# Performance work log

Hardware: AMD Instinct MI355X
Metric: run time of the kernel (lower is better)

The kernel has to match this reference:

```python
import jax, jax.numpy as jnp
import numpy as np

B, LENGTH, D, IN = 32, 32, 384, 384
NCELLS = LENGTH * (LENGTH + 1) // 2  # 528

def _offsets():
    off = np.zeros(LENGTH, dtype=np.int64)
    for lvl in range(1, LENGTH):
        off[lvl] = off[lvl - 1] + (LENGTH - (lvl - 1))
    return off

_OFF = _offsets()

def _inside_index(level):
    Ls = LENGTH - level
    pos = np.arange(Ls)[:, None]
    k = np.arange(level)[None, :]
    left = _OFF[k] + pos                      # span (k, pos)
    right = _OFF[level - k - 1] + pos + k + 1  # span (level-k-1, pos+k+1)
    return jnp.asarray(left), jnp.asarray(right)

def _outside_index(level):
    Ls = LENGTH - level
    N = LENGTH - level - 1  # constant #contexts per position
    par = np.zeros((Ls, N), dtype=np.int64)
    sib = np.zeros((Ls, N), dtype=np.int64)
    for pos in range(Ls):
        j = 0
        for s in range(LENGTH - pos - level - 1):  # node is left child
            par[pos, j] = _OFF[level + s + 1] + pos
            sib[pos, j] = _OFF[s] + pos + level + 1
            j += 1
        for s in range(pos):  # node is right child
            par[pos, j] = _OFF[level + s + 1] + pos - s - 1
            sib[pos, j] = _OFF[s] + pos - s - 1
            j += 1
    return jnp.asarray(par), jnp.asarray(sib)

def sigma_h(x):
    return x * jnp.tanh(jnp.sqrt(jax.nn.sigmoid(x)))

def layer_norm(x, g, b, eps=1e-5):
    mu = x.mean(-1, keepdims=True)
    var = ((x - mu) ** 2).mean(-1, keepdims=True)
    return (x - mu) * jax.lax.rsqrt(var + eps) * g + b

def compose(l, r, W0, W1, B0, W2, B1):
    h = sigma_h(l @ W0 + r @ W1 + B0)
    return sigma_h(h @ W2 + B1)

def bilinear(u, v, M):
    return jnp.einsum('blnd,de,blne->bln', u, M, v)[..., None]

def setup_inputs() -> dict:
    key = jax.random.key(0)
    ks = jax.random.split(key, 16)
    sc = 1.0 / np.sqrt(D)
    mk = lambda k, shp: (jax.random.normal(k, shp, dtype=jnp.float32) * sc)
    inp = {
        'x': jax.random.normal(ks[0], (B, LENGTH, IN), dtype=jnp.float32),
        'leaf_W': mk(ks[1], (IN, D)), 'leaf_b': jnp.zeros((D,), jnp.float32),
        'in_ln_g': jnp.ones((D,), jnp.float32), 'in_ln_b': jnp.zeros((D,), jnp.float32),
        'out_ln_g': jnp.ones((D,), jnp.float32), 'out_ln_b': jnp.zeros((D,), jnp.float32),
        'root_h': jax.random.normal(ks[2], (D,), dtype=jnp.float32) * 0.02,
        'in_bi': mk(ks[3], (D, D)), 'out_bi': mk(ks[4], (D, D)),
        'in_W0': mk(ks[5], (D, D)), 'in_W1': mk(ks[6], (D, D)),
        'in_B0': jnp.zeros((D,), jnp.float32),
        'in_W2': mk(ks[7], (D, D)), 'in_B1': jnp.zeros((D,), jnp.float32),
        'out_W0': mk(ks[8], (D, D)), 'out_W1': mk(ks[9], (D, D)),
        'out_B0': jnp.zeros((D,), jnp.float32),
        'out_W2': mk(ks[10], (D, D)), 'out_B1': jnp.zeros((D,), jnp.float32),
    }
    return inp

def reference(x, leaf_W, leaf_b, in_ln_g, in_ln_b, out_ln_g, out_ln_b, root_h,
              in_bi, out_bi, in_W0, in_W1, in_B0, in_W2, in_B1,
              out_W0, out_W1, out_B0, out_W2, out_B1):
    # leaf transform
    h0 = layer_norm(sigma_h(x @ leaf_W + leaf_b), in_ln_g, in_ln_b)
    ih = jnp.zeros((B, NCELLS, D), x.dtype).at[:, :LENGTH].set(h0)
    is_ = jnp.zeros((B, NCELLS, 1), x.dtype)
    # inside pass (CKY chart, level-by-level)
    for level in range(1, LENGTH):
        li, ri = _inside_index(level)
        lh, rh = ih[:, li], ih[:, ri]   # [B, Ls, level, D]
        ls, rs = is_[:, li], is_[:, ri]
        sc = bilinear(lh, rh, in_bi) + ls + rs
        p = jax.nn.softmax(sc, axis=2)
        xc = compose(lh, rh, in_W0, in_W1, in_B0, in_W2, in_B1)
        hbar = layer_norm((p * xc).sum(2), in_ln_g, in_ln_b)
        sbar = (p * sc).sum(2)
        o = int(_OFF[level]); Ls = LENGTH - level
        ih = ih.at[:, o:o + Ls].set(hbar)
        is_ = is_.at[:, o:o + Ls].set(sbar)
    # outside pass
    oh = jnp.zeros((B, NCELLS, D), x.dtype)
    os_ = jnp.zeros((B, NCELLS, 1), x.dtype)
    root = layer_norm(jnp.broadcast_to(root_h, (B, 1, D)), out_ln_g, out_ln_b)
    oh = oh.at[:, -1:].set(root)
    for level in range(LENGTH - 2, -1, -1):
        pi, si = _outside_index(level)
        ph, sh = oh[:, pi], ih[:, si]   # parent outside / sibling inside
        ps, ss = os_[:, pi], is_[:, si]
        sc = bilinear(sh, ph, out_bi) + ss + ps
        p = jax.nn.softmax(sc, axis=2)
        xc = compose(ph, sh, out_W0, out_W1, out_B0, out_W2, out_B1)
        hbar = layer_norm((p * xc).sum(2), out_ln_g, out_ln_b)
        sbar = (p * sc).sum(2)
        o = int(_OFF[level]); Ls = LENGTH - level
        oh = oh.at[:, o:o + Ls].set(hbar)
        os_ = os_.at[:, o:o + Ls].set(sbar)
    return ih, is_, oh, os_
```

## Files before the change

### kernel.cpp

```cpp
#include <hip/hip_runtime.h>
#include <cstddef>

#define BDIM 32
#define LEN 32
#define DD 384
#define NCELLS 528

typedef _Float16 h16;
typedef __attribute__((ext_vector_type(8))) _Float16 v8h;
typedef __attribute__((ext_vector_type(4))) float v4f;

__device__ __forceinline__ int offf(int k) { return k * 32 - ((k * (k - 1)) >> 1); }
static inline int offh(int k) { return k * 32 - ((k * (k - 1)) >> 1); }

__device__ __forceinline__ float sigma_h_f(float x) {
  float s = 1.0f / (1.0f + __expf(-x));
  float r = sqrtf(s);
  float e2 = __expf(2.0f * r);
  float th = 1.0f - 2.0f / (e2 + 1.0f);
  return x * th;
}

__device__ __forceinline__ size_t rowbase(int r, int gLs, int gOff) {
  if (gLs == 0) return (size_t)r;
  int b = r / gLs;
  int p = r - b * gLs;
  return (size_t)b * NCELLS + gOff + p;
}

__global__ __launch_bounds__(256) void pack3_k(
    const float* __restrict__ w0, const float* __restrict__ w1,
    const float* __restrict__ bi, const float* __restrict__ ow1,
    const float* __restrict__ obi, const float* __restrict__ w2,
    const float* __restrict__ ow2, const float* __restrict__ ow0,
    const float* __restrict__ lw,
    float* __restrict__ WCt, float* __restrict__ W2t, float* __restrict__ OW2t,
    float* __restrict__ OW0t, float* __restrict__ LWt,
    float* __restrict__ isp, float* __restrict__ osp) {
  int i = blockIdx.x * 256 + threadIdx.x;
  if (i < 1920 * 384) {
    int n = i / 384, k = i - n * 384;
    int sel = n / 384, c = n - sel * 384;
    const float* src = sel == 0 ? w0 : sel == 1 ? w1 : sel == 2 ? bi
                       : sel == 3 ? ow1 : obi;
    WCt[i] = src[k * 384 + c];
  }
  if (i < 384 * 384) {
    int n = i / 384, k = i - n * 384;
    W2t[i]  = w2[k * 384 + n];
    OW2t[i] = ow2[k * 384 + n];
    OW0t[i] = ow0[k * 384 + n];
    LWt[i]  = lw[k * 384 + n];
  }
  if (i < BDIM * NCELLS) { isp[i] = 0.0f; osp[i] = 0.0f; }
}

__global__ __launch_bounds__(256) void gemm32s(
    const float* __restrict__ A, const float* __restrict__ Wt,
    const float* __restrict__ bias, float* __restrict__ C,
    int M, int N, int act, int gLs, int gOff) {
  __shared__ h16 Ah[64][40], Al[64][40];
  __shared__ h16 Bh[128][40], Bl[128][40];
  int tid = threadIdx.x;
  int w = tid >> 6, lane = tid & 63;
  int m0 = blockIdx.x * 64, n0 = blockIdx.y * 128;
  int r = lane & 15, q = lane >> 4;

  v4f acc[4][2];
#pragma unroll
  for (int i = 0; i < 4; ++i)
#pragma unroll
    for (int j = 0; j < 2; ++j) acc[i][j] = (v4f){0.f, 0.f, 0.f, 0.f};

  int sar = tid >> 2;
  int sak = (tid & 3) << 3;
  const float* Aptr = nullptr;
  if (m0 + sar < M) Aptr = A + rowbase(m0 + sar, gLs, gOff) * (size_t)DD;
  int sbc = tid >> 1;
  int sbk = (tid & 1) << 4;
  const float* Bptr = Wt + (size_t)(n0 + sbc) * DD;

  for (int k0 = 0; k0 < DD; k0 += 32) {
    float4 a0 = make_float4(0.f, 0.f, 0.f, 0.f), a1 = a0;
    if (Aptr) {
      a0 = *reinterpret_cast<const float4*>(Aptr + k0 + sak);
      a1 = *reinterpret_cast<const float4*>(Aptr + k0 + sak + 4);
    }
    float4 b0 = *reinterpret_cast<const float4*>(Bptr + k0 + sbk);
    float4 b1 = *reinterpret_cast<const float4*>(Bptr + k0 + sbk + 4);
    float4 b2 = *reinterpret_cast<const float4*>(Bptr + k0 + sbk + 8);
    float4 b3 = *reinterpret_cast<const float4*>(Bptr + k0 + sbk + 12);
    __syncthreads();
    {
      float av[8] = {a0.x, a0.y, a0.z, a0.w, a1.x, a1.y, a1.z, a1.w};
      v8h hi, lo;
#pragma unroll
      for (int t = 0; t < 8; ++t) {
        h16 h = (h16)av[t];
        hi[t] = h;
        lo[t] = (h16)(av[t] - (float)h);
      }
      *reinterpret_cast<v8h*>(&Ah[sar][sak]) = hi;
      *reinterpret_cast<v8h*>(&Al[sar][sak]) = lo;
    }
    {
      float bv[16] = {b0.x, b0.y, b0.z, b0.w, b1.x, b1.y, b1.z, b1.w,
                      b2.x, b2.y, b2.z, b2.w, b3.x, b3.y, b3.z, b3.w};
      v8h hi0, lo0, hi1, lo1;
#pragma unroll
      for (int t = 0; t < 8; ++t) {
        h16 h = (h16)bv[t];
        hi0[t] = h;
        lo0[t] = (h16)(bv[t] - (float)h);
      }
#pragma unroll
      for (int t = 0; t < 8; ++t) {
        h16 h = (h16)bv[8 + t];
        hi1[t] = h;
        lo1[t] = (h16)(bv[8 + t] - (float)h);
      }
      *reinterpret_cast<v8h*>(&Bh[sbc][sbk]) = hi0;
      *reinterpret_cast<v8h*>(&Bl[sbc][sbk]) = lo0;
      *reinterpret_cast<v8h*>(&Bh[sbc][sbk + 8]) = hi1;
      *reinterpret_cast<v8h*>(&Bl[sbc][sbk + 8]) = lo1;
    }
    __syncthreads();
    v8h afh[4], afl[4], bfh[2], bfl[2];
#pragma unroll
    for (int i = 0; i < 4; ++i) {
      afh[i] = *reinterpret_cast<const v8h*>(&Ah[i * 16 + r][q * 8]);
      afl[i] = *reinterpret_cast<const v8h*>(&Al[i * 16 + r][q * 8]);
    }
#pragma unroll
    for (int j = 0; j < 2; ++j) {
      bfh[j] = *reinterpret_cast<const v8h*>(&Bh[w * 32 + j * 16 + r][q * 8]);
      bfl[j] = *reinterpret_cast<const v8h*>(&Bl[w * 32 + j * 16 + r][q * 8]);
    }
#pragma unroll
    for (int i = 0; i < 4; ++i)
#pragma unroll
      for (int j = 0; j < 2; ++j) {
        acc[i][j] = __builtin_amdgcn_mfma_f32_16x16x32_f16(afl[i], bfh[j], acc[i][j], 0, 0, 0);
        acc[i][j] = __builtin_amdgcn_mfma_f32_16x16x32_f16(afh[i], bfl[j], acc[i][j], 0, 0, 0);
        acc[i][j] = __builtin_amdgcn_mfma_f32_16x16x32_f16(afh[i], bfh[j], acc[i][j], 0, 0, 0);
      }
  }

#pragma unroll
  for (int i = 0; i < 4; ++i) {
#pragma unroll
    for (int reg = 0; reg < 4; ++reg) {
      int rr = m0 + i * 16 + q * 4 + reg;
      if (rr >= M) continue;
      size_t cb = rowbase(rr, gLs, gOff) * (size_t)N;
#pragma unroll
      for (int j = 0; j < 2; ++j) {
        int col = n0 + w * 32 + j * 16 + r;
        float v = acc[i][j][reg];
        if (bias) v += bias[col];
        if (act) v = sigma_h_f(v);
        C[cb + col] = v;
      }
    }
  }
}

__global__ __launch_bounds__(256) void k1_in(
    const float* __restrict__ PC, const float* __restrict__ ihp,
    float* __restrict__ isp, float* __restrict__ H, float* __restrict__ Pw,
    const float* __restrict__ B0, int L, int Ls, int offL) {
  int g = blockIdx.x;
  int b = g / Ls, pos = g - b * Ls;
  int tid = threadIdx.x, lane = tid & 63, wv = tid >> 6;
  __shared__ float scs[32];
  size_t cb = (size_t)b * NCELLS;
  for (int n = wv; n < L; n += 4) {
    int lc = offf(n) + pos;
    int rc = offf(L - 1 - n) + pos + n + 1;
    const float* u = PC + (cb + lc) * 1920 + 768;
    const float* v = ihp + (cb + rc) * (size_t)DD;
    float s = 0.0f;
#pragma unroll
    for (int jj = 0; jj < 6; ++jj) s += u[lane + 64 * jj] * v[lane + 64 * jj];
#pragma unroll
    for (int o = 32; o; o >>= 1) s += __shfl_xor(s, o, 64);
    if (lane == 0) scs[n] = s + isp[cb + lc] + isp[cb + rc];
  }
  __syncthreads();
  if (wv == 0) {
    float v = (lane < L) ? scs[lane] : -3.0e38f;
    float m = v;
#pragma unroll
    for (int o = 32; o; o >>= 1) m = fmaxf(m, __shfl_xor(m, o, 64));
    float e = (lane < L) ? __expf(v - m) : 0.0f;
    float S = e;
#pragma unroll
    for (int o = 32; o; o >>= 1) S += __shfl_xor(S, o, 64);
    float pn = e / S;
    if (lane < L) Pw[(size_t)g * L + lane] = pn;
    float sb = (lane < L) ? pn * v : 0.0f;
#pragma unroll
    for (int o = 32; o; o >>= 1) sb += __shfl_xor(sb, o, 64);
    if (lane == 0) isp[cb + offL + pos] = sb;
  }
  for (int n = 0; n < L; ++n) {
    int lc = offf(n) + pos;
    int rc = offf(L - 1 - n) + pos + n + 1;
    const float* A0r = PC + (cb + lc) * 1920;
    const float* A1r = PC + (cb + rc) * 1920 + 384;
    float* hrow = H + ((size_t)g * L + n) * DD;
    for (int k = tid; k < DD; k += 256)
      hrow[k] = sigma_h_f(A0r[k] + A1r[k] + B0[k]);
  }
}

__global__ __launch_bounds__(256) void k1_out(
    const float* __restrict__ PC, const float* __restrict__ P0,
    const float* __restrict__ ohp, const float* __restrict__ isp,
    float* __restrict__ osp, float* __restrict__ H, float* __restrict__ Pw,
    const float* __restrict__ B0, int L, int Ls, int Nc, int offL) {
  int g = blockIdx.x;
  int b = g / Ls, pos = g - b * Ls;
  int tid = threadIdx.x, lane = tid & 63, wv = tid >> 6;
  __shared__ float scs[32];
  size_t cb = (size_t)b * NCELLS;
  int cnt0 = 31 - pos - L;
  for (int j = wv; j < Nc; j += 4) {
    int par, sib;
    if (j < cnt0) { par = offf(L + j + 1) + pos; sib = offf(j) + pos + L + 1; }
    else { int s2 = j - cnt0; par = offf(L + s2 + 1) + pos - s2 - 1; sib = offf(s2) + pos - s2 - 1; }
    const float* u = PC + (cb + sib) * 1920 + 1536;
    const float* v = ohp + (cb + par) * (size_t)DD;
    float s = 0.0f;
#pragma unroll
    for (int jj = 0; jj < 6; ++jj) s += u[lane + 64 * jj] * v[lane + 64 * jj];
#pragma unroll
    for (int o = 32; o; o >>= 1) s += __shfl_xor(s, o, 64);
    if (lane == 0) scs[j] = s + isp[cb + sib] + osp[cb + par];
  }
  __syncthreads();
  if (wv == 0) {
    float v = (lane < Nc) ? scs[lane] : -3.0e38f;
    float m = v;
#pragma unroll
    for (int o = 32; o; o >>= 1) m = fmaxf(m, __shfl_xor(m, o, 64));
    float e = (lane < Nc) ? __expf(v - m) : 0.0f;
    float S = e;
#pragma unroll
    for (int o = 32; o; o >>= 1) S += __shfl_xor(S, o, 64);
    float pn = e / S;
    if (lane < Nc) Pw[(size_t)g * Nc + lane] = pn;
    float sb = (lane < Nc) ? pn * v : 0.0f;
#pragma unroll
    for (int o = 32; o; o >>= 1) sb += __shfl_xor(sb, o, 64);
    if (lane == 0) osp[cb + offL + pos] = sb;
  }
  for (int j = 0; j < Nc; ++j) {
    int par, sib;
    if (j < cnt0) { par = offf(L + j + 1) + pos; sib = offf(j) + pos + L + 1; }
    else { int s2 = j - cnt0; par = offf(L + s2 + 1) + pos - s2 - 1; sib = offf(s2) + pos - s2 - 1; }
    const float* p0r = P0 + (cb + par) * (size_t)DD;
    const float* s1r = PC + (cb + sib) * 1920 + 1152;
    float* hrow = H + ((size_t)g * Nc + j) * DD;
    for (int k = tid; k < DD; k += 256)
      hrow[k] = sigma_h_f(p0r[k] + s1r[k] + B0[k]);
  }
}

__global__ __launch_bounds__(128) void k3_red_ln(
    const float* __restrict__ XC, const float* __restrict__ Pw,
    const float* __restrict__ lng, const float* __restrict__ lnb,
    float* __restrict__ outArr, int L, int Ls, int offL) {
  int g = blockIdx.x;
  int b = g / Ls, pos = g - b * Ls;
  int tid = threadIdx.x;
  float a0 = 0, a1 = 0, a2 = 0;
  const float* base = XC + (size_t)g * L * DD;
  for (int n = 0; n < L; ++n) {
    float pw = Pw ? Pw[(size_t)g * L + n] : 1.0f;
    const float* row = base + (size_t)n * DD;
    a0 += pw * row[tid];
    a1 += pw * row[tid + 128];
    a2 += pw * row[tid + 256];
  }
  int lane = tid & 63, wv = tid >> 6;
  float s = a0 + a1 + a2;
#pragma unroll
  for (int o = 32; o; o >>= 1) s += __shfl_xor(s, o, 64);
  __shared__ float r1[2], r2[2];
  if (lane == 0) r1[wv] = s;
  __syncthreads();
  float mean = (r1[0] + r1[1]) * (1.0f / 384.0f);
  float d0 = a0 - mean, d1 = a1 - mean, d2 = a2 - mean;
  float q = d0 * d0 + d1 * d1 + d2 * d2;
#pragma unroll
  for (int o = 32; o; o >>= 1) q += __shfl_xor(q, o, 64);
  if (lane == 0) r2[wv] = q;
  __syncthreads();
  float var = (r2[0] + r2[1]) * (1.0f / 384.0f);
  float inv = rsqrtf(var + 1e-5f);
  float* out = outArr + ((size_t)b * NCELLS + offL + pos) * DD;
  out[tid]       = d0 * inv * lng[tid]       + lnb[tid];
  out[tid + 128] = d1 * inv * lng[tid + 128] + lnb[tid + 128];
  out[tid + 256] = d2 * inv * lng[tid + 256] + lnb[tid + 256];
}

__global__ __launch_bounds__(384) void root_k(
    const float* __restrict__ rooth, const float* __restrict__ lng,
    const float* __restrict__ lnb, const float* __restrict__ W0,
    float* __restrict__ ohp, float* __restrict__ P0) {
  int tid = threadIdx.x;
  int lane = tid & 63, wv = tid >> 6;
  __shared__ float rl[384];
  __shared__ float r1[6], r2[6];
  float x = rooth[tid];
  float s = x;
#pragma unroll
  for (int o = 32; o; o >>= 1) s += __shfl_xor(s, o, 64);
  if (lane == 0) r1[wv] = s;
  __syncthreads();
  float mean = (r1[0] + r1[1] + r1[2] + r1[3] + r1[4] + r1[5]) * (1.0f / 384.0f);
  float d = x - mean;
  float q = d * d;
#pragma unroll
  for (int o = 32; o; o >>= 1) q += __shfl_xor(q, o, 64);
  if (lane == 0) r2[wv] = q;
  __syncthreads();
  float var = (r2[0] + r2[1] + r2[2] + r2[3] + r2[4] + r2[5]) * (1.0f / 384.0f);
  float inv = rsqrtf(var + 1e-5f);
  float v = d * inv * lng[tid] + lnb[tid];
  rl[tid] = v;
  __syncthreads();
  for (int b2 = 0; b2 < BDIM; ++b2)
    ohp[((size_t)b2 * NCELLS + 527) * DD + tid] = v;
  float acc = 0.0f;
  for (int d2 = 0; d2 < 384; ++d2) acc += rl[d2] * W0[(size_t)d2 * 384 + tid];
  for (int b2 = 0; b2 < BDIM; ++b2)
    P0[((size_t)b2 * NCELLS + 527) * DD + tid] = acc;
}

extern "C" void kernel_launch(void* const* d_in, const int* in_sizes, int n_in,
                              void* d_out, int out_size, void* d_ws, size_t ws_size,
                              hipStream_t stream) {
  const float* x        = (const float*)d_in[0];
  const float* leaf_W   = (const float*)d_in[1];
  const float* leaf_b   = (const float*)d_in[2];
  const float* in_ln_g  = (const float*)d_in[3];
  const float* in_ln_b  = (const float*)d_in[4];
  const float* out_ln_g = (const float*)d_in[5];
  const float* out_ln_b = (const float*)d_in[6];
  const float* root_h   = (const float*)d_in[7];
  const float* in_bi    = (const float*)d_in[8];
  const float* out_bi   = (const float*)d_in[9];
  const float* in_W0    = (const float*)d_in[10];
  const float* in_W1    = (const float*)d_in[11];
  const float* in_B0    = (const float*)d_in[12];
  const float* in_W2    = (const float*)d_in[13];
  const float* in_B1    = (const float*)d_in[14];
  const float* out_W0   = (const float*)d_in[15];
  const float* out_W1   = (const float*)d_in[16];
  const float* out_B0   = (const float*)d_in[17];
  const float* out_W2   = (const float*)d_in[18];
  const float* out_B1   = (const float*)d_in[19];

  float* ih  = (float*)d_out;
  float* isp = ih + (size_t)BDIM * NCELLS * DD;
  float* oh  = isp + (size_t)BDIM * NCELLS;
  float* osp = oh + (size_t)BDIM * NCELLS * DD;

  float* PC   = (float*)d_ws;
  float* P0   = PC + (size_t)BDIM * NCELLS * 1920;
  float* XCb  = P0 + (size_t)BDIM * NCELLS * 384;
  float* Hbuf = XCb + (size_t)31744 * 384;
  float* Pw   = Hbuf + (size_t)31744 * 384;
  float* WCt  = Pw + 31744;
  float* W2t  = WCt + (size_t)1920 * 384;
  float* OW2t = W2t + (size_t)384 * 384;
  float* OW0t = OW2t + (size_t)384 * 384;
  float* LWt  = OW0t + (size_t)384 * 384;

  pack3_k<<<2880, 256, 0, stream>>>(in_W0, in_W1, in_bi, out_W1, out_bi,
                                    in_W2, out_W2, out_W0, leaf_W,
                                    WCt, W2t, OW2t, OW0t, LWt, isp, osp);

  gemm32s<<<dim3(16, 3), 256, 0, stream>>>(x, LWt, leaf_b, XCb, 1024, 384, 1, 0, 0);
  k3_red_ln<<<1024, 128, 0, stream>>>(XCb, nullptr, in_ln_g, in_ln_b, ih, 1, 32, 0);
  gemm32s<<<dim3(16, 15), 256, 0, stream>>>(ih, WCt, nullptr, PC, 1024, 1920, 0, 32, 0);

  for (int L = 1; L < LEN; ++L) {
    int Ls = LEN - L, G = BDIM * Ls, M = G * L, off = offh(L);
    k1_in<<<G, 256, 0, stream>>>(PC, ih, isp, Hbuf, Pw, in_B0, L, Ls, off);
    gemm32s<<<dim3((M + 63) / 64, 3), 256, 0, stream>>>(Hbuf, W2t, in_B1, XCb, M, 384, 1, 0, 0);
    k3_red_ln<<<G, 128, 0, stream>>>(XCb, Pw, in_ln_g, in_ln_b, ih, L, Ls, off);
    gemm32s<<<dim3((G + 63) / 64, 15), 256, 0, stream>>>(ih, WCt, nullptr, PC, G, 1920, 0, Ls, off);
  }

  root_k<<<1, 384, 0, stream>>>(root_h, out_ln_g, out_ln_b, out_W0, oh, P0);

  for (int L = LEN - 2; L >= 0; --L) {
    int Ls = LEN - L, Nc = LEN - 1 - L, G = BDIM * Ls, M = G * Nc, off = offh(L);
    k1_out<<<G, 256, 0, stream>>>(PC, P0, oh, isp, osp, Hbuf, Pw, out_B0, L, Ls, Nc, off);
    gemm32s<<<dim3((M + 63) / 64, 3), 256, 0, stream>>>(Hbuf, OW2t, out_B1, XCb, M, 384, 1, 0, 0);
    k3_red_ln<<<G, 128, 0, stream>>>(XCb, Pw, out_ln_g, out_ln_b, oh, Nc, Ls, off);
    if (L > 0)
      gemm32s<<<dim3((G + 63) / 64, 3), 256, 0, stream>>>(oh, OW0t, nullptr, P0, G, 384, 0, Ls, off);
  }
}
```

Baseline: 5.101 ms.

## Pre-split GEMM operands into fp16 hi/lo pairs at producer kernels

Weights, the input x, the hidden activations and the layer-norm outputs are now split into fp16 high and low parts once, in the kernels that produce them, and stored in separate buffers. The GEMM kernel then loads the split halves directly instead of loading fp32 and converting in every tile. This removes per-tile conversion work and redundant weight conversion across the many GEMM launches, and halves nothing in bytes read (hi plus lo equals fp32 size). The cost is extra global writes of the split copies in producer kernels and a new workspace layout that reuses the H buffers for x and compacted layer-norm outputs.

Result: faster. 4.927 ms (-3.4%).

```diff
diff --git a/kernel.cpp b/kernel.cpp
--- a/kernel.cpp
+++ b/kernel.cpp
@@ -28,14 +28,23 @@
   return (size_t)b * NCELLS + gOff + p;
 }
 
+__device__ __forceinline__ void split16(float v, h16& h, h16& l) {
+  h = (h16)v;
+  l = (h16)(v - (float)h);
+}
+
 __global__ __launch_bounds__(256) void pack3_k(
     const float* __restrict__ w0, const float* __restrict__ w1,
     const float* __restrict__ bi, const float* __restrict__ ow1,
     const float* __restrict__ obi, const float* __restrict__ w2,
     const float* __restrict__ ow2, const float* __restrict__ ow0,
-    const float* __restrict__ lw,
-    float* __restrict__ WCt, float* __restrict__ W2t, float* __restrict__ OW2t,
-    float* __restrict__ OW0t, float* __restrict__ LWt,
+    const float* __restrict__ lw, const float* __restrict__ x,
+    h16* __restrict__ WCth, h16* __restrict__ WCtl,
+    h16* __restrict__ W2th, h16* __restrict__ W2tl,
+    h16* __restrict__ OW2th, h16* __restrict__ OW2tl,
+    h16* __restrict__ OW0th, h16* __restrict__ OW0tl,
+    h16* __restrict__ LWth, h16* __restrict__ LWtl,
+    h16* __restrict__ xh, h16* __restrict__ xl,
     float* __restrict__ isp, float* __restrict__ osp) {
   int i = blockIdx.x * 256 + threadIdx.x;
   if (i < 1920 * 384) {
@@ -43,20 +52,28 @@
     int sel = n / 384, c = n - sel * 384;
     const float* src = sel == 0 ? w0 : sel == 1 ? w1 : sel == 2 ? bi
                        : sel == 3 ? ow1 : obi;
-    WCt[i] = src[k * 384 + c];
+    float v = src[k * 384 + c];
+    h16 h, l; split16(v, h, l);
+    WCth[i] = h; WCtl[i] = l;
   }
   if (i < 384 * 384) {
     int n = i / 384, k = i - n * 384;
-    W2t[i]  = w2[k * 384 + n];
-    OW2t[i] = ow2[k * 384 + n];
-    OW0t[i] = ow0[k * 384 + n];
-    LWt[i]  = lw[k * 384 + n];
+    h16 h, l;
+    split16(w2[k * 384 + n], h, l);  W2th[i] = h;  W2tl[i] = l;
+    split16(ow2[k * 384 + n], h, l); OW2th[i] = h; OW2tl[i] = l;
+    split16(ow0[k * 384 + n], h, l); OW0th[i] = h; OW0tl[i] = l;
+    split16(lw[k * 384 + n], h, l);  LWth[i] = h;  LWtl[i] = l;
+  }
+  if (i < 1024 * 384) {
+    h16 h, l; split16(x[i], h, l);
+    xh[i] = h; xl[i] = l;
   }
   if (i < BDIM * NCELLS) { isp[i] = 0.0f; osp[i] = 0.0f; }
 }
 
-__global__ __launch_bounds__(256) void gemm32s(
-    const float* __restrict__ A, const float* __restrict__ Wt,
+__global__ __launch_bounds__(256) void gemmh(
+    const h16* __restrict__ Ahp, const h16* __restrict__ Alp,
+    const h16* __restrict__ Bth, const h16* __restrict__ Btl,
     const float* __restrict__ bias, float* __restrict__ C,
     int M, int N, int act, int gLs, int gOff) {
   __shared__ h16 Ah[64][40], Al[64][40];
@@ -74,56 +91,36 @@
 
   int sar = tid >> 2;
   int sak = (tid & 3) << 3;
-  const float* Aptr = nullptr;
-  if (m0 + sar < M) Aptr = A + rowbase(m0 + sar, gLs, gOff) * (size_t)DD;
+  const h16* Aph = nullptr;
+  const h16* Apl = nullptr;
+  if (m0 + sar < M) {
+    size_t rb = (size_t)(m0 + sar) * DD;
+    Aph = Ahp + rb + sak;
+    Apl = Alp + rb + sak;
+  }
   int sbc = tid >> 1;
   int sbk = (tid & 1) << 4;
-  const float* Bptr = Wt + (size_t)(n0 + sbc) * DD;
+  const h16* Bph = Bth + (size_t)(n0 + sbc) * DD + sbk;
+  const h16* Bpl = Btl + (size_t)(n0 + sbc) * DD + sbk;
 
   for (int k0 = 0; k0 < DD; k0 += 32) {
-    float4 a0 = make_float4(0.f, 0.f, 0.f, 0.f), a1 = a0;
-    if (Aptr) {
-      a0 = *reinterpret_cast<const float4*>(Aptr + k0 + sak);
-      a1 = *reinterpret_cast<const float4*>(Aptr + k0 + sak + 4);
-    }
-    float4 b0 = *reinterpret_cast<const float4*>(Bptr + k0 + sbk);
-    float4 b1 = *reinterpret_cast<const float4*>(Bptr + k0 + sbk + 4);
-    float4 b2 = *reinterpret_cast<const float4*>(Bptr + k0 + sbk + 8);
-    float4 b3 = *reinterpret_cast<const float4*>(Bptr + k0 + sbk + 12);
+    v8h a_h = (v8h){0.f, 0.f, 0.f, 0.f, 0.f, 0.f, 0.f, 0.f};
+    v8h a_l = a_h;
+    if (Aph) {
+      a_h = *reinterpret_cast<const v8h*>(Aph + k0);
+      a_l = *reinterpret_cast<const v8h*>(Apl + k0);
+    }
+    v8h b_h0 = *reinterpret_cast<const v8h*>(Bph + k0);
+    v8h b_h1 = *reinterpret_cast<const v8h*>(Bph + k0 + 8);
+    v8h b_l0 = *reinterpret_cast<const v8h*>(Bpl + k0);
+    v8h b_l1 = *reinterpret_cast<const v8h*>(Bpl + k0 + 8);
     __syncthreads();
-    {
-      float av[8] = {a0.x, a0.y, a0.z, a0.w, a1.x, a1.y, a1.z, a1.w};
-      v8h hi, lo;
-#pragma unroll
-      for (int t = 0; t < 8; ++t) {
-        h16 h = (h16)av[t];
-        hi[t] = h;
-        lo[t] = (h16)(av[t] - (float)h);
-      }
-      *reinterpret_cast<v8h*>(&Ah[sar][sak]) = hi;
-      *reinterpret_cast<v8h*>(&Al[sar][sak]) = lo;
-    }
-    {
-      float bv[16] = {b0.x, b0.y, b0.z, b0.w, b1.x, b1.y, b1.z, b1.w,
-                      b2.x, b2.y, b2.z, b2.w, b3.x, b3.y, b3.z, b3.w};
-      v8h hi0, lo0, hi1, lo1;
-#pragma unroll
-      for (int t = 0; t < 8; ++t) {
-        h16 h = (h16)bv[t];
-        hi0[t] = h;
-        lo0[t] = (h16)(bv[t] - (float)h);
-      }
-#pragma unroll
-      for (int t = 0; t < 8; ++t) {
-        h16 h = (h16)bv[8 + t];
-        hi1[t] = h;
-        lo1[t] = (h16)(bv[8 + t] - (float)h);
-      }
-      *reinterpret_cast<v8h*>(&Bh[sbc][sbk]) = hi0;
-      *reinterpret_cast<v8h*>(&Bl[sbc][sbk]) = lo0;
-      *reinterpret_cast<v8h*>(&Bh[sbc][sbk + 8]) = hi1;
-      *reinterpret_cast<v8h*>(&Bl[sbc][sbk + 8]) = lo1;
-    }
+    *reinterpret_cast<v8h*>(&Ah[sar][sak]) = a_h;
+    *reinterpret_cast<v8h*>(&Al[sar][sak]) = a_l;
+    *reinterpret_cast<v8h*>(&Bh[sbc][sbk]) = b_h0;
+    *reinterpret_cast<v8h*>(&Bh[sbc][sbk + 8]) = b_h1;
+    *reinterpret_cast<v8h*>(&Bl[sbc][sbk]) = b_l0;
+    *reinterpret_cast<v8h*>(&Bl[sbc][sbk + 8]) = b_l1;
     __syncthreads();
     v8h afh[4], afl[4], bfh[2], bfl[2];
 #pragma unroll
@@ -167,8 +164,9 @@
 
 __global__ __launch_bounds__(256) void k1_in(
     const float* __restrict__ PC, const float* __restrict__ ihp,
-    float* __restrict__ isp, float* __restrict__ H, float* __restrict__ Pw,
-    const float* __restrict__ B0, int L, int Ls, int offL) {
+    float* __restrict__ isp, h16* __restrict__ Hh, h16* __restrict__ Hl,
+    float* __restrict__ Pw, const float* __restrict__ B0,
+    int L, int Ls, int offL) {
   int g = blockIdx.x;
   int b = g / Ls, pos = g - b * Ls;
   int tid = threadIdx.x, lane = tid & 63, wv = tid >> 6;
@@ -208,17 +206,22 @@
     int rc = offf(L - 1 - n) + pos + n + 1;
     const float* A0r = PC + (cb + lc) * 1920;
     const float* A1r = PC + (cb + rc) * 1920 + 384;
-    float* hrow = H + ((size_t)g * L + n) * DD;
-    for (int k = tid; k < DD; k += 256)
-      hrow[k] = sigma_h_f(A0r[k] + A1r[k] + B0[k]);
+    size_t hb = ((size_t)g * L + n) * DD;
+    for (int k = tid; k < DD; k += 256) {
+      float v = sigma_h_f(A0r[k] + A1r[k] + B0[k]);
+      h16 h = (h16)v;
+      Hh[hb + k] = h;
+      Hl[hb + k] = (h16)(v - (float)h);
+    }
   }
 }
 
 __global__ __launch_bounds__(256) void k1_out(
     const float* __restrict__ PC, const float* __restrict__ P0,
     const float* __restrict__ ohp, const float* __restrict__ isp,
-    float* __restrict__ osp, float* __restrict__ H, float* __restrict__ Pw,
-    const float* __restrict__ B0, int L, int Ls, int Nc, int offL) {
+    float* __restrict__ osp, h16* __restrict__ Hh, h16* __restrict__ Hl,
+    float* __restrict__ Pw, const float* __restrict__ B0,
+    int L, int Ls, int Nc, int offL) {
   int g = blockIdx.x;
   int b = g / Ls, pos = g - b * Ls;
   int tid = threadIdx.x, lane = tid & 63, wv = tid >> 6;
@@ -261,16 +264,21 @@
     else { int s2 = j - cnt0; par = offf(L + s2 + 1) + pos - s2 - 1; sib = offf(s2) + pos - s2 - 1; }
     const float* p0r = P0 + (cb + par) * (size_t)DD;
     const float* s1r = PC + (cb + sib) * 1920 + 1152;
-    float* hrow = H + ((size_t)g * Nc + j) * DD;
-    for (int k = tid; k < DD; k += 256)
-      hrow[k] = sigma_h_f(p0r[k] + s1r[k] + B0[k]);
+    size_t hb = ((size_t)g * Nc + j) * DD;
+    for (int k = tid; k < DD; k += 256) {
+      float v = sigma_h_f(p0r[k] + s1r[k] + B0[k]);
+      h16 h = (h16)v;
+      Hh[hb + k] = h;
+      Hl[hb + k] = (h16)(v - (float)h);
+    }
   }
 }
 
 __global__ __launch_bounds__(128) void k3_red_ln(
     const float* __restrict__ XC, const float* __restrict__ Pw,
     const float* __restrict__ lng, const float* __restrict__ lnb,
-    float* __restrict__ outArr, int L, int Ls, int offL) {
+    float* __restrict__ outArr, h16* __restrict__ outh, h16* __restrict__ outl,
+    int L, int Ls, int offL) {
   int g = blockIdx.x;
   int b = g / Ls, pos = g - b * Ls;
   int tid = threadIdx.x;
@@ -299,10 +307,19 @@
   __syncthreads();
   float var = (r2[0] + r2[1]) * (1.0f / 384.0f);
   float inv = rsqrtf(var + 1e-5f);
-  float* out = outArr + ((size_t)b * NCELLS + offL + pos) * DD;
-  out[tid]       = d0 * inv * lng[tid]       + lnb[tid];
-  out[tid + 128] = d1 * inv * lng[tid + 128] + lnb[tid + 128];
-  out[tid + 256] = d2 * inv * lng[tid + 256] + lnb[tid + 256];
+  size_t ob = ((size_t)b * NCELLS + offL + pos) * DD;
+  float* out = outArr + ob;
+  float v0 = d0 * inv * lng[tid]       + lnb[tid];
+  float v1 = d1 * inv * lng[tid + 128] + lnb[tid + 128];
+  float v2 = d2 * inv * lng[tid + 256] + lnb[tid + 256];
+  out[tid]       = v0;
+  out[tid + 128] = v1;
+  out[tid + 256] = v2;
+  size_t sb = (size_t)g * DD;
+  h16 h;
+  h = (h16)v0; outh[sb + tid]       = h; outl[sb + tid]       = (h16)(v0 - (float)h);
+  h = (h16)v1; outh[sb + tid + 128] = h; outl[sb + tid + 128] = (h16)(v1 - (float)h);
+  h = (h16)v2; outh[sb + tid + 256] = h; outl[sb + tid + 256] = (h16)(v2 - (float)h);
 }
 
 __global__ __launch_bounds__(384) void root_k(
@@ -368,41 +385,53 @@
   float* oh  = isp + (size_t)BDIM * NCELLS;
   float* osp = oh + (size_t)BDIM * NCELLS * DD;
 
-  float* PC   = (float*)d_ws;
-  float* P0   = PC + (size_t)BDIM * NCELLS * 1920;
-  float* XCb  = P0 + (size_t)BDIM * NCELLS * 384;
-  float* Hbuf = XCb + (size_t)31744 * 384;
-  float* Pw   = Hbuf + (size_t)31744 * 384;
-  float* WCt  = Pw + 31744;
-  float* W2t  = WCt + (size_t)1920 * 384;
-  float* OW2t = W2t + (size_t)384 * 384;
-  float* OW0t = OW2t + (size_t)384 * 384;
-  float* LWt  = OW0t + (size_t)384 * 384;
+  float* PC  = (float*)d_ws;
+  float* P0  = PC + (size_t)32440320;
+  float* XCb = P0 + (size_t)6488064;
+  float* Pw  = XCb + (size_t)12189696;
+  h16* Hh    = (h16*)(Pw + 31744);
+  h16* Hl    = Hh + (size_t)12189696;
+  h16* WCth  = Hl + (size_t)12189696;
+  h16* WCtl  = WCth + (size_t)737280;
+  h16* W2th  = WCtl + (size_t)737280;
+  h16* W2tl  = W2th + (size_t)147456;
+  h16* OW2th = W2tl + (size_t)147456;
+  h16* OW2tl = OW2th + (size_t)147456;
+  h16* OW0th = OW2tl + (size_t)147456;
+  h16* OW0tl = OW0th + (size_t)147456;
+  h16* LWth  = OW0tl + (size_t)147456;
+  h16* LWtl  = LWth + (size_t)147456;
+  h16* xh = Hh;
+  h16* xl = Hl;
+  h16* Ch = Hh + (size_t)16384 * DD;
+  h16* Cl = Hl + (size_t)16384 * DD;
 
   pack3_k<<<2880, 256, 0, stream>>>(in_W0, in_W1, in_bi, out_W1, out_bi,
-                                    in_W2, out_W2, out_W0, leaf_W,
-                                    WCt, W2t, OW2t, OW0t, LWt, isp, osp);
-
-  gemm32s<<<dim3(16, 3), 256, 0, stream>>>(x, LWt, leaf_b, XCb, 1024, 384, 1, 0, 0);
-  k3_red_ln<<<1024, 128, 0, stream>>>(XCb, nullptr, in_ln_g, in_ln_b, ih, 1, 32, 0);
-  gemm32s<<<dim3(16, 15), 256, 0, stream>>>(ih, WCt, nullptr, PC, 1024, 1920, 0, 32, 0);
+                                    in_W2, out_W2, out_W0, leaf_W, x,
+                                    WCth, WCtl, W2th, W2tl, OW2th, OW2tl,
+                                    OW0th, OW0tl, LWth, LWtl, xh, xl,
+                                    isp, osp);
+
+  gemmh<<<dim3(16, 3), 256, 0, stream>>>(xh, xl, LWth, LWtl, leaf_b, XCb, 1024, 384, 1, 0, 0);
+  k3_red_ln<<<1024, 128, 0, stream>>>(XCb, nullptr, in_ln_g, in_ln_b, ih, Ch, Cl, 1, 32, 0);
+  gemmh<<<dim3(16, 15), 256, 0, stream>>>(Ch, Cl, WCth, WCtl, nullptr, PC, 1024, 1920, 0, 32, 0);
 
   for (int L = 1; L < LEN; ++L) {
     int Ls = LEN - L, G = BDIM * Ls, M = G * L, off = offh(L);
-    k1_in<<<G, 256, 0, stream>>>(PC, ih, isp, Hbuf, Pw, in_B0, L, Ls, off);
-    gemm32s<<<dim3((M + 63) / 64, 3), 256, 0, stream>>>(Hbuf, W2t, in_B1, XCb, M, 384, 1, 0, 0);
-    k3_red_ln<<<G, 128, 0, stream>>>(XCb, Pw, in_ln_g, in_ln_b, ih, L, Ls, off);
-    gemm32s<<<dim3((G + 63) / 64, 15), 256, 0, stream>>>(ih, WCt, nullptr, PC, G, 1920, 0, Ls, off);
+    k1_in<<<G, 256, 0, stream>>>(PC, ih, isp, Hh, Hl, Pw, in_B0, L, Ls, off);
+    gemmh<<<dim3((M + 63) / 64, 3), 256, 0, stream>>>(Hh, Hl, W2th, W2tl, in_B1, XCb, M, 384, 1, 0, 0);
+    k3_red_ln<<<G, 128, 0, stream>>>(XCb, Pw, in_ln_g, in_ln_b, ih, Ch, Cl, L, Ls, off);
+    gemmh<<<dim3((G + 63) / 64, 15), 256, 0, stream>>>(Ch, Cl, WCth, WCtl, nullptr, PC, G, 1920, 0, Ls, off);
   }
 
   root_k<<<1, 384, 0, stream>>>(root_h, out_ln_g, out_ln_b, out_W0, oh, P0);
 
   for (int L = LEN - 2; L >= 0; --L) {
     int Ls = LEN - L, Nc = LEN - 1 - L, G = BDIM * Ls, M = G * Nc, off = offh(L);
-    k1_out<<<G, 256, 0, stream>>>(PC, P0, oh, isp, osp, Hbuf, Pw, out_B0, L, Ls, Nc, off);
-    gemm32s<<<dim3((M + 63) / 64, 3), 256, 0, stream>>>(Hbuf, OW2t, out_B1, XCb, M, 384, 1, 0, 0);
-    k3_red_ln<<<G, 128, 0, stream>>>(XCb, Pw, out_ln_g, out_ln_b, oh, Nc, Ls, off);
+    k1_out<<<G, 256, 0, stream>>>(PC, P0, oh, isp, osp, Hh, Hl, Pw, out_B0, L, Ls, Nc, off);
+    gemmh<<<dim3((M + 63) / 64, 3), 256, 0, stream>>>(Hh, Hl, OW2th, OW2tl, out_B1, XCb, M, 384, 1, 0, 0);
+    k3_red_ln<<<G, 128, 0, stream>>>(XCb, Pw, out_ln_g, out_ln_b, oh, Ch, Cl, Nc, Ls, off);
     if (L > 0)
-      gemm32s<<<dim3((G + 63) / 64, 3), 256, 0, stream>>>(oh, OW0t, nullptr, P0, G, 384, 0, Ls, off);
-  }
-}
+      gemmh<<<dim3((G + 63) / 64, 3), 256, 0, stream>>>(Ch, Cl, OW0th, OW0tl, nullptr, P0, G, 384, 0, Ls, off);
+  }
+}
```
